# Kernel optimization log

Measured on AMD Instinct MI355X. Metric: run time of the kernel, lower is better.

Reference implementation:

```python
import jax, jax.numpy as jnp
import numpy as np

N = 50000   # nodes
E = 800000  # directed edges
D = 128     # input_channels


def _kaiming(key, shape):
    fan_in = shape[0]
    return jax.random.normal(key, shape, jnp.float32) * np.float32(np.sqrt(2.0 / fan_in))


def setup_inputs():
    key = jax.random.key(0)
    ks = jax.random.split(key, 8)
    x = jax.random.normal(ks[0], (N, D), jnp.float32)
    edge_index = jax.random.randint(ks[1], (2, E), 0, N, dtype=jnp.int32)
    return {
        "x": x,
        "edge_index": edge_index,
        "W_in": _kaiming(ks[2], (D, D)),      "b_in": jnp.zeros((D,), jnp.float32),
        "W1": _kaiming(ks[3], (D, 2 * D)),    "b1": jnp.zeros((2 * D,), jnp.float32),
        "W2": _kaiming(ks[4], (2 * D, D)),    "b2": jnp.zeros((D,), jnp.float32),
        "W3": _kaiming(ks[5], (D, D // 2)),   "b3": jnp.zeros((D // 2,), jnp.float32),
        "W_out": _kaiming(ks[6], (D // 2, 1)), "b_out": jnp.zeros((1,), jnp.float32),
    }


def _gcn_conv(x, src, dst, W, b, n):
    """PyG GCNConv: add self-loops, symmetric D^-1/2 (A+I) D^-1/2 normalization."""
    h = x @ W  # [n, out]
    loop = jnp.arange(n, dtype=src.dtype)
    s = jnp.concatenate([src, loop])  # message sources (x_j)
    d = jnp.concatenate([dst, loop])  # aggregation targets (x_i)
    deg = jax.ops.segment_sum(jnp.ones_like(d, jnp.float32), d, num_segments=n)
    dis = jnp.where(deg > 0, jax.lax.rsqrt(jnp.maximum(deg, 1.0)), 0.0)
    norm = dis[s] * dis[d]  # [E+n]
    msg = h[s] * norm[:, None]  # gather + scale
    out = jax.ops.segment_sum(msg, d, num_segments=n)  # scatter-add
    return out + b


def reference(x, edge_index, W_in, b_in, W1, b1, W2, b2, W3, b3, W_out, b_out):
    src, dst = edge_index[0], edge_index[1]
    n = x.shape[0]
    lrelu = lambda t: jax.nn.leaky_relu(t, 0.01)
    # dropout in eval mode (identity)
    h = lrelu(x @ W_in + b_in)
    h = lrelu(_gcn_conv(h, src, dst, W1, b1, n))
    h = lrelu(_gcn_conv(h, src, dst, W2, b2, n))
    h = lrelu(_gcn_conv(h, src, dst, W3, b3, n))
    return h @ W_out + b_out  # [n, 1]
```

## Files before the change

### kernel.cpp

```cpp
#include <hip/hip_runtime.h>


#define LRELU(v) ((v) > 0.f ? (v) : 0.01f * (v))

typedef __attribute__((ext_vector_type(8))) _Float16 half8;
typedef __attribute__((ext_vector_type(8))) float float8;
typedef __attribute__((ext_vector_type(4))) float floatx4;

constexpr int CAP = 64;

__global__ __launch_bounds__(256) void k_prep(const int* __restrict__ src,
                                              const int* __restrict__ dst,
                                              int* __restrict__ cnt,
                                              unsigned short* __restrict__ pad,
                                              const float* __restrict__ W_in,
                                              const float* __restrict__ W1,
                                              const float* __restrict__ W2,
                                              const float* __restrict__ W3,
                                              _Float16* __restrict__ wt_in,
                                              _Float16* __restrict__ wt1,
                                              _Float16* __restrict__ wt2,
                                              _Float16* __restrict__ wt3,
                                              int E, int PR) {
  const int b = blockIdx.x;
  const int tid = threadIdx.x;
  if (b < 128) {
    const int m = b >> 5;
    const int blk = b & 31;
    const int idx = blk * 256 + tid;
    if (m == 0) {
      for (int i = idx; i < 128 * 128; i += 8192) {
        const int k = i >> 7, f = i & 127;
        wt_in[f * 128 + k] = (_Float16)W_in[i];
      }
    } else if (m == 1) {
      for (int i = idx; i < 128 * 256; i += 8192) {
        const int k = i >> 8, f = i & 255;
        wt1[f * 128 + k] = (_Float16)W1[i];
      }
    } else if (m == 2) {
      for (int i = idx; i < 256 * 128; i += 8192) {
        const int k = i >> 7, f = i & 127;
        wt2[f * 256 + k] = (_Float16)W2[i];
      }
    } else {
      for (int i = idx; i < 128 * 64; i += 8192) {
        const int k = i >> 6, f = i & 63;
        wt3[f * 128 + k] = (_Float16)W3[i];
      }
    }
  } else {
    const int bb = b - 128;
    const int range = bb & 7;
    const int chunk = bb >> 3;
    const int e = chunk * 256 + tid;
    if (e < E) {
      const int d = dst[e];
      if (d / PR == range) {
        const int pos = atomicAdd(&cnt[d], 1);
        if (pos < CAP) pad[(long)d * CAP + pos] = (unsigned short)src[e];
      }
    }
  }
}

template <int K, int F, int EPI, typename IT>
__global__ __launch_bounds__(256) void k_gemm(const IT* __restrict__ X,
                                              const _Float16* __restrict__ Wt,
                                              const float* __restrict__ b,
                                              const int* __restrict__ cnt,
                                              _Float16* __restrict__ out, int M) {
  constexpr int TM = 64;
  constexpr int PAD = 8;
  constexpr int LK = K + PAD;
  constexpr int CW = F / 4;
  constexpr int NT = CW / 16;
  constexpr int NK = K / 32;
  __shared__ _Float16 xs[TM * LK];

  const int m0 = blockIdx.x * TM;
  const int tid = threadIdx.x;
  const int w = tid >> 6;
  const int lane = tid & 63;
  const int m = lane & 15;
  const int q = lane >> 4;

  half8 breg[NT][NK];
#pragma unroll
  for (int t = 0; t < NT; ++t)
#pragma unroll
    for (int kc = 0; kc < NK; ++kc)
      breg[t][kc] =
          *(const half8*)&Wt[(long)(w * CW + t * 16 + m) * K + kc * 32 + q * 8];

  constexpr int CPR = K / 8;
  for (int idx = tid; idx < TM * CPR; idx += 256) {
    const int row = idx / CPR;
    const int kk = idx % CPR;
    const int g = m0 + row;
    half8 h = (half8)(_Float16)0.f;
    if (g < M) {
      if constexpr (sizeof(IT) == 4) {
        const float4* p = (const float4*)&X[(long)g * K + kk * 8];
        float4 a = p[0], c = p[1];
        h[0] = (_Float16)a.x; h[1] = (_Float16)a.y;
        h[2] = (_Float16)a.z; h[3] = (_Float16)a.w;
        h[4] = (_Float16)c.x; h[5] = (_Float16)c.y;
        h[6] = (_Float16)c.z; h[7] = (_Float16)c.w;
      } else {
        h = *(const half8*)&X[(long)g * K + kk * 8];
      }
    }
    *(half8*)&xs[row * LK + kk * 8] = h;
  }
  __syncthreads();

  floatx4 acc[4][NT];
#pragma unroll
  for (int rt = 0; rt < 4; ++rt)
#pragma unroll
    for (int t = 0; t < NT; ++t) acc[rt][t] = (floatx4){0.f, 0.f, 0.f, 0.f};

#pragma unroll
  for (int kc = 0; kc < NK; ++kc) {
    half8 af[4];
#pragma unroll
    for (int rt = 0; rt < 4; ++rt)
      af[rt] = *(const half8*)&xs[(rt * 16 + m) * LK + kc * 32 + q * 8];
#pragma unroll
    for (int rt = 0; rt < 4; ++rt)
#pragma unroll
      for (int t = 0; t < NT; ++t)
        acc[rt][t] = __builtin_amdgcn_mfma_f32_16x16x32_f16(af[rt], breg[t][kc],
                                                            acc[rt][t], 0, 0, 0);
  }

#pragma unroll
  for (int rt = 0; rt < 4; ++rt) {
#pragma unroll
    for (int r = 0; r < 4; ++r) {
      const int row = m0 + rt * 16 + q * 4 + r;
      if (row < M) {
        const float dv = rsqrtf((float)cnt[row] + 1.0f);
#pragma unroll
        for (int t = 0; t < NT; ++t) {
          const int col = w * CW + t * 16 + m;
          float v = acc[rt][t][r];
          if constexpr (EPI == 0) { v += b[col]; v = LRELU(v); v *= dv; }
          if constexpr (EPI == 2) { v *= dv; }
          out[(long)row * F + col] = (_Float16)v;
        }
      }
    }
  }
}

__global__ __launch_bounds__(256) void k_gemm2x(const _Float16* __restrict__ X,
                                                const _Float16* __restrict__ Wt1,
                                                const float* __restrict__ b1,
                                                const _Float16* __restrict__ Wt2,
                                                const int* __restrict__ cnt,
                                                _Float16* __restrict__ out,
                                                int M) {
  constexpr int TM = 64;
  constexpr int LK1 = 128 + 8;
  constexpr int LK2 = 256 + 8;
  __shared__ _Float16 xs[TM * LK1];
  __shared__ _Float16 ys[TM * LK2];

  const int m0 = blockIdx.x * TM;
  const int tid = threadIdx.x;
  const int w = tid >> 6;
  const int lane = tid & 63;
  const int m = lane & 15;
  const int q = lane >> 4;

  for (int idx = tid; idx < TM * 16; idx += 256) {
    const int row = idx >> 4;
    const int kk = idx & 15;
    const int g = m0 + row;
    half8 h = (half8)(_Float16)0.f;
    if (g < M) h = *(const half8*)&X[(long)g * 128 + kk * 8];
    *(half8*)&xs[row * LK1 + kk * 8] = h;
  }

  half8 breg1[4][4];
#pragma unroll
  for (int t = 0; t < 4; ++t)
#pragma unroll
    for (int kc = 0; kc < 4; ++kc)
      breg1[t][kc] =
          *(const half8*)&Wt1[(long)(w * 64 + t * 16 + m) * 128 + kc * 32 + q * 8];

  __syncthreads();

  floatx4 acc1[4][4];
#pragma unroll
  for (int rt = 0; rt < 4; ++rt)
#pragma unroll
    for (int t = 0; t < 4; ++t) acc1[rt][t] = (floatx4){0.f, 0.f, 0.f, 0.f};

#pragma unroll
  for (int kc = 0; kc < 4; ++kc) {
    half8 af[4];
#pragma unroll
    for (int rt = 0; rt < 4; ++rt)
      af[rt] = *(const half8*)&xs[(rt * 16 + m) * LK1 + kc * 32 + q * 8];
#pragma unroll
    for (int rt = 0; rt < 4; ++rt)
#pragma unroll
      for (int t = 0; t < 4; ++t)
        acc1[rt][t] = __builtin_amdgcn_mfma_f32_16x16x32_f16(af[rt], breg1[t][kc],
                                                             acc1[rt][t], 0, 0, 0);
  }

#pragma unroll
  for (int rt = 0; rt < 4; ++rt) {
#pragma unroll
    for (int r = 0; r < 4; ++r) {
      const int row = rt * 16 + q * 4 + r;
#pragma unroll
      for (int t = 0; t < 4; ++t) {
        const int col = w * 64 + t * 16 + m;
        float v = acc1[rt][t][r] + b1[col];
        ys[row * LK2 + col] = (_Float16)LRELU(v);
      }
    }
  }

  half8 breg2[2][8];
#pragma unroll
  for (int t = 0; t < 2; ++t)
#pragma unroll
    for (int kc = 0; kc < 8; ++kc)
      breg2[t][kc] =
          *(const half8*)&Wt2[(long)(w * 32 + t * 16 + m) * 256 + kc * 32 + q * 8];

  __syncthreads();

  floatx4 acc2[4][2];
#pragma unroll
  for (int rt = 0; rt < 4; ++rt)
#pragma unroll
    for (int t = 0; t < 2; ++t) acc2[rt][t] = (floatx4){0.f, 0.f, 0.f, 0.f};

#pragma unroll
  for (int kc = 0; kc < 8; ++kc) {
    half8 af[4];
#pragma unroll
    for (int rt = 0; rt < 4; ++rt)
      af[rt] = *(const half8*)&ys[(rt * 16 + m) * LK2 + kc * 32 + q * 8];
#pragma unroll
    for (int rt = 0; rt < 4; ++rt)
#pragma unroll
      for (int t = 0; t < 2; ++t)
        acc2[rt][t] = __builtin_amdgcn_mfma_f32_16x16x32_f16(af[rt], breg2[t][kc],
                                                             acc2[rt][t], 0, 0, 0);
  }

#pragma unroll
  for (int rt = 0; rt < 4; ++rt) {
#pragma unroll
    for (int r = 0; r < 4; ++r) {
      const int row = m0 + rt * 16 + q * 4 + r;
      if (row < M) {
        const float dv = rsqrtf((float)cnt[row] + 1.0f);
#pragma unroll
        for (int t = 0; t < 2; ++t) {
          const int col = w * 32 + t * 16 + m;
          out[(long)row * 128 + col] = (_Float16)(acc2[rt][t][r] * dv);
        }
      }
    }
  }
}

template <int F, int MODE>
__global__ __launch_bounds__(256) void k_agg(const _Float16* __restrict__ G,
                                             const unsigned short* __restrict__ pad,
                                             const int* __restrict__ cnt,
                                             const float* __restrict__ b,
                                             const float* __restrict__ Wout,
                                             const float* __restrict__ bout,
                                             void* __restrict__ out, int N) {
  const int w = threadIdx.x >> 6;
  const int lane = threadIdx.x & 63;
  const int c = lane & 7;
  const int j = lane >> 3;
  const int n = j >> 2;
  const int jj = j & 3;
  const int i0 = blockIdx.x * 8 + w * 2;
  int i = i0 + n;
  const bool valid = (i < N);
  if (!valid) i = N - 1;
  const int col0 = (F == 128) ? ((int)blockIdx.y << 6) : 0;

  const _Float16* gbase = G + col0 + c * 8;
  const int cn = min(cnt[i], CAP);
  const unsigned short* plist = pad + (long)i * CAP;

  float8 acc = {0.f, 0.f, 0.f, 0.f, 0.f, 0.f, 0.f, 0.f};
  if (jj == 0)
    acc = __builtin_convertvector(*(const half8*)(gbase + (long)i * F), float8);
  for (int e = jj; e < cn; e += 4) {
    const int s = plist[e];
    acc += __builtin_convertvector(*(const half8*)(gbase + (long)s * F), float8);
  }
#pragma unroll
  for (int k = 0; k < 8; ++k) {
    acc[k] += __shfl_xor(acc[k], 8);
    acc[k] += __shfl_xor(acc[k], 16);
  }

  const float dv = rsqrtf((float)cnt[i] + 1.0f);
  if constexpr (MODE == 2) {
    float p = 0.f;
#pragma unroll
    for (int k = 0; k < 8; ++k) {
      const int col = c * 8 + k;
      float v = acc[k] * dv + b[col];
      v = LRELU(v);
      p += v * Wout[col];
    }
    p += __shfl_xor(p, 1);
    p += __shfl_xor(p, 2);
    p += __shfl_xor(p, 4);
    if (valid && jj == 0 && c == 0) ((float*)out)[i] = p + bout[0];
  } else {
    if (valid && jj == 0) {
      half8 hv;
#pragma unroll
      for (int k = 0; k < 8; ++k) {
        float v = acc[k] * dv;
        if constexpr (MODE == 1) { v += b[col0 + c * 8 + k]; v = LRELU(v); }
        hv[k] = (_Float16)v;
      }
      *(half8*)&((_Float16*)out)[(long)i * F + col0 + c * 8] = hv;
    }
  }
}


extern "C" void kernel_launch(void* const* d_in, const int* in_sizes, int n_in,
                              void* d_out, int out_size, void* d_ws, size_t ws_size,
                              hipStream_t stream) {
  const float* x     = (const float*)d_in[0];
  const int* eidx    = (const int*)d_in[1];
  const float* W_in  = (const float*)d_in[2];
  const float* b_in  = (const float*)d_in[3];
  const float* W1    = (const float*)d_in[4];
  const float* b1    = (const float*)d_in[5];
  const float* W2    = (const float*)d_in[6];
  const float* b2    = (const float*)d_in[7];
  const float* W3    = (const float*)d_in[8];
  const float* b3    = (const float*)d_in[9];
  const float* W_out = (const float*)d_in[10];
  const float* b_out = (const float*)d_in[11];
  float* out = (float*)d_out;

  const int N = in_sizes[0] / 128;
  const int E = in_sizes[1] / 2;
  const int* src = eidx;
  const int* dst = eidx + E;
  const int PR = (N + 7) / 8;

  size_t off = 0;
  char* base = (char*)d_ws;
  auto alloc = [&](size_t bytes) -> void* {
    void* p = base + off;
    off = (off + bytes + 255) & ~(size_t)255;
    return p;
  };
  int* cnt            = (int*)alloc((size_t)N * sizeof(int));
  unsigned short* pad = (unsigned short*)alloc((size_t)N * CAP * 2);
  _Float16* wt_in     = (_Float16*)alloc((size_t)128 * 128 * 2);
  _Float16* wt1       = (_Float16*)alloc((size_t)256 * 128 * 2);
  _Float16* wt2       = (_Float16*)alloc((size_t)128 * 256 * 2);
  _Float16* wt3       = (_Float16*)alloc((size_t)64 * 128 * 2);
  _Float16* buf1      = (_Float16*)alloc((size_t)N * 128 * 2);
  _Float16* buf2      = (_Float16*)alloc((size_t)N * 128 * 2);
  _Float16* buf3      = (_Float16*)alloc((size_t)N * 64 * 2);

  hipMemsetAsync(cnt, 0, (size_t)N * sizeof(int), stream);

  const int gE = (E + 255) / 256;
  const int gRows = (N + 63) / 64;
  const int gAggP = (N + 7) / 8;

  k_prep<<<128 + 8 * gE, 256, 0, stream>>>(src, dst, cnt, pad,
                                           W_in, W1, W2, W3,
                                           wt_in, wt1, wt2, wt3, E, PR);

  k_gemm<128, 128, 0, float><<<gRows, 256, 0, stream>>>(x, wt_in, b_in, cnt,
                                                        buf1, N);
  k_agg<128, 0><<<dim3(gAggP, 2), 256, 0, stream>>>(buf1, pad, cnt, nullptr,
                                                    nullptr, nullptr, buf2, N);
  k_gemm2x<<<gRows, 256, 0, stream>>>(buf2, wt1, b1, wt2, cnt, buf1, N);
  k_agg<128, 1><<<dim3(gAggP, 2), 256, 0, stream>>>(buf1, pad, cnt, b2,
                                                    nullptr, nullptr, buf2, N);
  k_gemm<128, 64, 2, _Float16><<<gRows, 256, 0, stream>>>(buf2, wt3, nullptr,
                                                          cnt, buf3, N);
  k_agg<64, 2><<<gAggP, 256, 0, stream>>>(buf3, pad, cnt, b3,
                                          W_out, b_out, out, N);
}
```

Before: 273.4 us.

## Fuse whole GCN pipeline into one persistent cooperative kernel with grid syncs

```diff
diff --git a/kernel.cpp b/kernel.cpp
--- a/kernel.cpp
+++ b/kernel.cpp
@@ -1,4 +1,7 @@
 #include <hip/hip_runtime.h>
+#include <hip/hip_cooperative_groups.h>
+
+namespace cg = cooperative_groups;
 
 
 #define LRELU(v) ((v) > 0.f ? (v) : 0.01f * (v))
@@ -8,6 +11,470 @@
 typedef __attribute__((ext_vector_type(4))) float floatx4;
 
 constexpr int CAP = 64;
+
+template <int K, int F, int EPI, typename IT>
+__device__ __forceinline__ void gemm_tile(const IT* __restrict__ X,
+                                          const _Float16* __restrict__ Wt,
+                                          const float* __restrict__ bias,
+                                          const int* __restrict__ cnt,
+                                          _Float16* __restrict__ out, int M,
+                                          int tile, _Float16* __restrict__ xs) {
+  constexpr int TM = 64;
+  constexpr int PAD = 8;
+  constexpr int LK = K + PAD;
+  constexpr int CW = F / 4;
+  constexpr int NT = CW / 16;
+  constexpr int NK = K / 32;
+
+  const int m0 = tile * TM;
+  const int tid = threadIdx.x;
+  const int w = tid >> 6;
+  const int lane = tid & 63;
+  const int m = lane & 15;
+  const int q = lane >> 4;
+
+  half8 breg[NT][NK];
+#pragma unroll
+  for (int t = 0; t < NT; ++t)
+#pragma unroll
+    for (int kc = 0; kc < NK; ++kc)
+      breg[t][kc] =
+          *(const half8*)&Wt[(long)(w * CW + t * 16 + m) * K + kc * 32 + q * 8];
+
+  constexpr int CPR = K / 8;
+  for (int idx = tid; idx < TM * CPR; idx += 256) {
+    const int row = idx / CPR;
+    const int kk = idx % CPR;
+    const int g = m0 + row;
+    half8 h = (half8)(_Float16)0.f;
+    if (g < M) {
+      if constexpr (sizeof(IT) == 4) {
+        const float4* p = (const float4*)&X[(long)g * K + kk * 8];
+        float4 a = p[0], cc = p[1];
+        h[0] = (_Float16)a.x; h[1] = (_Float16)a.y;
+        h[2] = (_Float16)a.z; h[3] = (_Float16)a.w;
+        h[4] = (_Float16)cc.x; h[5] = (_Float16)cc.y;
+        h[6] = (_Float16)cc.z; h[7] = (_Float16)cc.w;
+      } else {
+        h = *(const half8*)&X[(long)g * K + kk * 8];
+      }
+    }
+    *(half8*)&xs[row * LK + kk * 8] = h;
+  }
+  __syncthreads();
+
+  floatx4 acc[4][NT];
+#pragma unroll
+  for (int rt = 0; rt < 4; ++rt)
+#pragma unroll
+    for (int t = 0; t < NT; ++t) acc[rt][t] = (floatx4){0.f, 0.f, 0.f, 0.f};
+
+#pragma unroll
+  for (int kc = 0; kc < NK; ++kc) {
+    half8 af[4];
+#pragma unroll
+    for (int rt = 0; rt < 4; ++rt)
+      af[rt] = *(const half8*)&xs[(rt * 16 + m) * LK + kc * 32 + q * 8];
+#pragma unroll
+    for (int rt = 0; rt < 4; ++rt)
+#pragma unroll
+      for (int t = 0; t < NT; ++t)
+        acc[rt][t] = __builtin_amdgcn_mfma_f32_16x16x32_f16(af[rt], breg[t][kc],
+                                                            acc[rt][t], 0, 0, 0);
+  }
+
+#pragma unroll
+  for (int rt = 0; rt < 4; ++rt) {
+#pragma unroll
+    for (int r = 0; r < 4; ++r) {
+      const int row = m0 + rt * 16 + q * 4 + r;
+      if (row < M) {
+        float dv = 1.f;
+        if constexpr (EPI == 0 || EPI == 2) dv = rsqrtf((float)cnt[row] + 1.0f);
+#pragma unroll
+        for (int t = 0; t < NT; ++t) {
+          const int col = w * CW + t * 16 + m;
+          float v = acc[rt][t][r];
+          if constexpr (EPI == 0) { v += bias[col]; v = LRELU(v); v *= dv; }
+          if constexpr (EPI == 1) { v += bias[col]; v = LRELU(v); }
+          if constexpr (EPI == 2) { v *= dv; }
+          out[(long)row * F + col] = (_Float16)v;
+        }
+      }
+    }
+  }
+}
+
+__device__ __forceinline__ void gemm2x_tile(const _Float16* __restrict__ X,
+                                            const _Float16* __restrict__ Wt1,
+                                            const float* __restrict__ b1,
+                                            const _Float16* __restrict__ Wt2,
+                                            const int* __restrict__ cnt,
+                                            _Float16* __restrict__ out, int M,
+                                            int tile, _Float16* __restrict__ xs,
+                                            _Float16* __restrict__ ys) {
+  constexpr int LK1 = 128 + 8;
+  constexpr int LK2 = 256 + 8;
+
+  const int m0 = tile * 64;
+  const int tid = threadIdx.x;
+  const int w = tid >> 6;
+  const int lane = tid & 63;
+  const int m = lane & 15;
+  const int q = lane >> 4;
+
+  for (int idx = tid; idx < 64 * 16; idx += 256) {
+    const int row = idx >> 4;
+    const int kk = idx & 15;
+    const int g = m0 + row;
+    half8 h = (half8)(_Float16)0.f;
+    if (g < M) h = *(const half8*)&X[(long)g * 128 + kk * 8];
+    *(half8*)&xs[row * LK1 + kk * 8] = h;
+  }
+
+  half8 breg1[4][4];
+#pragma unroll
+  for (int t = 0; t < 4; ++t)
+#pragma unroll
+    for (int kc = 0; kc < 4; ++kc)
+      breg1[t][kc] =
+          *(const half8*)&Wt1[(long)(w * 64 + t * 16 + m) * 128 + kc * 32 + q * 8];
+
+  __syncthreads();
+
+  floatx4 acc1[4][4];
+#pragma unroll
+  for (int rt = 0; rt < 4; ++rt)
+#pragma unroll
+    for (int t = 0; t < 4; ++t) acc1[rt][t] = (floatx4){0.f, 0.f, 0.f, 0.f};
+
+#pragma unroll
+  for (int kc = 0; kc < 4; ++kc) {
+    half8 af[4];
+#pragma unroll
+    for (int rt = 0; rt < 4; ++rt)
+      af[rt] = *(const half8*)&xs[(rt * 16 + m) * LK1 + kc * 32 + q * 8];
+#pragma unroll
+    for (int rt = 0; rt < 4; ++rt)
+#pragma unroll
+      for (int t = 0; t < 4; ++t)
+        acc1[rt][t] = __builtin_amdgcn_mfma_f32_16x16x32_f16(af[rt], breg1[t][kc],
+                                                             acc1[rt][t], 0, 0, 0);
+  }
+
+#pragma unroll
+  for (int rt = 0; rt < 4; ++rt) {
+#pragma unroll
+    for (int r = 0; r < 4; ++r) {
+      const int row = rt * 16 + q * 4 + r;
+#pragma unroll
+      for (int t = 0; t < 4; ++t) {
+        const int col = w * 64 + t * 16 + m;
+        float v = acc1[rt][t][r] + b1[col];
+        ys[row * LK2 + col] = (_Float16)LRELU(v);
+      }
+    }
+  }
+
+  half8 breg2[2][8];
+#pragma unroll
+  for (int t = 0; t < 2; ++t)
+#pragma unroll
+    for (int kc = 0; kc < 8; ++kc)
+      breg2[t][kc] =
+          *(const half8*)&Wt2[(long)(w * 32 + t * 16 + m) * 256 + kc * 32 + q * 8];
+
+  __syncthreads();
+
+  floatx4 acc2[4][2];
+#pragma unroll
+  for (int rt = 0; rt < 4; ++rt)
+#pragma unroll
+    for (int t = 0; t < 2; ++t) acc2[rt][t] = (floatx4){0.f, 0.f, 0.f, 0.f};
+
+#pragma unroll
+  for (int kc = 0; kc < 8; ++kc) {
+    half8 af[4];
+#pragma unroll
+    for (int rt = 0; rt < 4; ++rt)
+      af[rt] = *(const half8*)&ys[(rt * 16 + m) * LK2 + kc * 32 + q * 8];
+#pragma unroll
+    for (int rt = 0; rt < 4; ++rt)
+#pragma unroll
+      for (int t = 0; t < 2; ++t)
+        acc2[rt][t] = __builtin_amdgcn_mfma_f32_16x16x32_f16(af[rt], breg2[t][kc],
+                                                             acc2[rt][t], 0, 0, 0);
+  }
+
+#pragma unroll
+  for (int rt = 0; rt < 4; ++rt) {
+#pragma unroll
+    for (int r = 0; r < 4; ++r) {
+      const int row = m0 + rt * 16 + q * 4 + r;
+      if (row < M) {
+        const float dv = rsqrtf((float)cnt[row] + 1.0f);
+#pragma unroll
+        for (int t = 0; t < 2; ++t) {
+          const int col = w * 32 + t * 16 + m;
+          out[(long)row * 128 + col] = (_Float16)(acc2[rt][t][r] * dv);
+        }
+      }
+    }
+  }
+}
+
+__device__ __forceinline__ void agg128_pre(const _Float16* __restrict__ G,
+                                           const unsigned short* __restrict__ pad,
+                                           const int* __restrict__ cnt,
+                                           _Float16* __restrict__ out, int N,
+                                           int nb) {
+  const int w = threadIdx.x >> 6;
+  const int lane = threadIdx.x & 63;
+  const int c = lane & 15;
+  const int jj = lane >> 4;
+  const int ng = (N + 3) >> 2;
+  for (int t = blockIdx.x; t < ng; t += nb) {
+    int i = t * 4 + w;
+    const bool valid = (i < N);
+    if (!valid) i = N - 1;
+    const int cni = cnt[i];
+    const int cn = min(cni, CAP);
+    const float dvi = rsqrtf((float)cni + 1.f);
+    const _Float16* gb = G + c * 8;
+    const unsigned short* pl = pad + (long)i * CAP;
+
+    float8 a0 = {0.f, 0.f, 0.f, 0.f, 0.f, 0.f, 0.f, 0.f};
+    float8 a1 = a0, a2 = a0, a3 = a0;
+    if (jj == 0) {
+      float8 f = __builtin_convertvector(*(const half8*)(gb + (long)i * 128), float8);
+#pragma unroll
+      for (int k = 0; k < 8; ++k) a0[k] = f[k] * dvi;
+    }
+    int e = jj;
+    for (; e + 12 < cn; e += 16) {
+      const int s0 = pl[e], s1 = pl[e + 4], s2 = pl[e + 8], s3 = pl[e + 12];
+      const float d0 = rsqrtf((float)cnt[s0] + 1.f);
+      const float d1 = rsqrtf((float)cnt[s1] + 1.f);
+      const float d2 = rsqrtf((float)cnt[s2] + 1.f);
+      const float d3 = rsqrtf((float)cnt[s3] + 1.f);
+      float8 f0 = __builtin_convertvector(*(const half8*)(gb + (long)s0 * 128), float8);
+      float8 f1 = __builtin_convertvector(*(const half8*)(gb + (long)s1 * 128), float8);
+      float8 f2 = __builtin_convertvector(*(const half8*)(gb + (long)s2 * 128), float8);
+      float8 f3 = __builtin_convertvector(*(const half8*)(gb + (long)s3 * 128), float8);
+#pragma unroll
+      for (int k = 0; k < 8; ++k) {
+        a0[k] += f0[k] * d0;
+        a1[k] += f1[k] * d1;
+        a2[k] += f2[k] * d2;
+        a3[k] += f3[k] * d3;
+      }
+    }
+    for (; e < cn; e += 4) {
+      const int s = pl[e];
+      const float d = rsqrtf((float)cnt[s] + 1.f);
+      float8 f = __builtin_convertvector(*(const half8*)(gb + (long)s * 128), float8);
+#pragma unroll
+      for (int k = 0; k < 8; ++k) a0[k] += f[k] * d;
+    }
+#pragma unroll
+    for (int k = 0; k < 8; ++k) a0[k] += a1[k] + a2[k] + a3[k];
+#pragma unroll
+    for (int k = 0; k < 8; ++k) {
+      a0[k] += __shfl_xor(a0[k], 16);
+      a0[k] += __shfl_xor(a0[k], 32);
+    }
+    if (valid && jj == 0) {
+      half8 hv;
+#pragma unroll
+      for (int k = 0; k < 8; ++k) hv[k] = (_Float16)(a0[k] * dvi);
+      *(half8*)&out[(long)i * 128 + c * 8] = hv;
+    }
+  }
+}
+
+__device__ __forceinline__ void agg128_post(const _Float16* __restrict__ G,
+                                            const unsigned short* __restrict__ pad,
+                                            const int* __restrict__ cnt,
+                                            const float* __restrict__ bias,
+                                            _Float16* __restrict__ out, int N,
+                                            int nb) {
+  const int w = threadIdx.x >> 6;
+  const int lane = threadIdx.x & 63;
+  const int c = lane & 15;
+  const int jj = lane >> 4;
+  const int ng = (N + 3) >> 2;
+  for (int t = blockIdx.x; t < ng; t += nb) {
+    int i = t * 4 + w;
+    const bool valid = (i < N);
+    if (!valid) i = N - 1;
+    const int cni = cnt[i];
+    const int cn = min(cni, CAP);
+    const float dvi = rsqrtf((float)cni + 1.f);
+    const _Float16* gb = G + c * 8;
+    const unsigned short* pl = pad + (long)i * CAP;
+
+    float8 a0 = {0.f, 0.f, 0.f, 0.f, 0.f, 0.f, 0.f, 0.f};
+    float8 a1 = a0, a2 = a0, a3 = a0;
+    if (jj == 0)
+      a0 = __builtin_convertvector(*(const half8*)(gb + (long)i * 128), float8);
+    int e = jj;
+    for (; e + 12 < cn; e += 16) {
+      const int s0 = pl[e], s1 = pl[e + 4], s2 = pl[e + 8], s3 = pl[e + 12];
+      a0 += __builtin_convertvector(*(const half8*)(gb + (long)s0 * 128), float8);
+      a1 += __builtin_convertvector(*(const half8*)(gb + (long)s1 * 128), float8);
+      a2 += __builtin_convertvector(*(const half8*)(gb + (long)s2 * 128), float8);
+      a3 += __builtin_convertvector(*(const half8*)(gb + (long)s3 * 128), float8);
+    }
+    for (; e < cn; e += 4) {
+      const int s = pl[e];
+      a0 += __builtin_convertvector(*(const half8*)(gb + (long)s * 128), float8);
+    }
+    a0 += a1 + a2 + a3;
+#pragma unroll
+    for (int k = 0; k < 8; ++k) {
+      a0[k] += __shfl_xor(a0[k], 16);
+      a0[k] += __shfl_xor(a0[k], 32);
+    }
+    if (valid && jj == 0) {
+      half8 hv;
+#pragma unroll
+      for (int k = 0; k < 8; ++k) {
+        float v = a0[k] * dvi + bias[c * 8 + k];
+        hv[k] = (_Float16)LRELU(v);
+      }
+      *(half8*)&out[(long)i * 128 + c * 8] = hv;
+    }
+  }
+}
+
+__device__ __forceinline__ void agg_final(const _Float16* __restrict__ G,
+                                          const unsigned short* __restrict__ pad,
+                                          const int* __restrict__ cnt,
+                                          const float* __restrict__ b3,
+                                          const float* __restrict__ Wout,
+                                          const float* __restrict__ bout,
+                                          float* __restrict__ out, int N, int nb) {
+  const int w = threadIdx.x >> 6;
+  const int lane = threadIdx.x & 63;
+  const int c = lane & 7;
+  const int j = lane >> 3;
+  const int n = j >> 2;
+  const int jj = j & 3;
+  const int ng = (N + 7) >> 3;
+  for (int t = blockIdx.x; t < ng; t += nb) {
+    int i = t * 8 + w * 2 + n;
+    const bool valid = (i < N);
+    if (!valid) i = N - 1;
+    const int cni = cnt[i];
+    const int cn = min(cni, CAP);
+    const float dvi = rsqrtf((float)cni + 1.f);
+    const _Float16* gb = G + c * 8;
+    const unsigned short* pl = pad + (long)i * CAP;
+
+    float8 a0 = {0.f, 0.f, 0.f, 0.f, 0.f, 0.f, 0.f, 0.f};
+    float8 a1 = a0;
+    if (jj == 0)
+      a0 = __builtin_convertvector(*(const half8*)(gb + (long)i * 64), float8);
+    int e = jj;
+    for (; e + 4 < cn; e += 8) {
+      const int s0 = pl[e], s1 = pl[e + 4];
+      a0 += __builtin_convertvector(*(const half8*)(gb + (long)s0 * 64), float8);
+      a1 += __builtin_convertvector(*(const half8*)(gb + (long)s1 * 64), float8);
+    }
+    if (e < cn)
+      a0 += __builtin_convertvector(*(const half8*)(gb + (long)pl[e] * 64), float8);
+    a0 += a1;
+#pragma unroll
+    for (int k = 0; k < 8; ++k) {
+      a0[k] += __shfl_xor(a0[k], 8);
+      a0[k] += __shfl_xor(a0[k], 16);
+    }
+    float p = 0.f;
+#pragma unroll
+    for (int k = 0; k < 8; ++k) {
+      const int col = c * 8 + k;
+      float v = a0[k] * dvi + b3[col];
+      v = LRELU(v);
+      p += v * Wout[col];
+    }
+    p += __shfl_xor(p, 1);
+    p += __shfl_xor(p, 2);
+    p += __shfl_xor(p, 4);
+    if (valid && jj == 0 && c == 0) out[i] = p + bout[0];
+  }
+}
+
+__global__ __launch_bounds__(256, 2) void k_gcn(
+    const float* __restrict__ x, const int* __restrict__ src,
+    const int* __restrict__ dst, const float* __restrict__ W_in,
+    const float* __restrict__ b_in, const float* __restrict__ W1,
+    const float* __restrict__ b1, const float* __restrict__ W2,
+    const float* __restrict__ b2, const float* __restrict__ W3,
+    const float* __restrict__ b3, const float* __restrict__ W_out,
+    const float* __restrict__ b_out, float* __restrict__ out,
+    int* __restrict__ cnt, unsigned short* __restrict__ pad,
+    _Float16* __restrict__ wt_in, _Float16* __restrict__ wt1,
+    _Float16* __restrict__ wt2, _Float16* __restrict__ wt3,
+    _Float16* __restrict__ buf1, _Float16* __restrict__ buf2,
+    _Float16* __restrict__ buf3, int N, int E, int PR) {
+  __shared__ _Float16 smem[64 * 136 + 64 * 264];
+  cg::grid_group grid = cg::this_grid();
+  const int nb = gridDim.x;
+  const int b = blockIdx.x;
+  const int tid = threadIdx.x;
+  const int gid = b * 256 + tid;
+  const int gs = nb * 256;
+
+  for (int i = gid; i < N; i += gs) cnt[i] = 0;
+  for (int i = gid; i < 128 * 128; i += gs)
+    wt_in[(i & 127) * 128 + (i >> 7)] = (_Float16)W_in[i];
+  for (int i = gid; i < 128 * 256; i += gs)
+    wt1[(i & 255) * 128 + (i >> 8)] = (_Float16)W1[i];
+  for (int i = gid; i < 256 * 128; i += gs)
+    wt2[(i & 127) * 256 + (i >> 7)] = (_Float16)W2[i];
+  for (int i = gid; i < 128 * 64; i += gs)
+    wt3[(i & 63) * 128 + (i >> 6)] = (_Float16)W3[i];
+  grid.sync();
+
+  const int gE = (E + 255) >> 8;
+  for (int ch = b; ch < 8 * gE; ch += nb) {
+    const int range = ch & 7;
+    const int e = (ch >> 3) * 256 + tid;
+    if (e < E) {
+      const int d = dst[e];
+      if ((unsigned)(d - range * PR) < (unsigned)PR) {
+        const int pos = atomicAdd(&cnt[d], 1);
+        if (pos < CAP) pad[(long)d * CAP + pos] = (unsigned short)src[e];
+      }
+    }
+  }
+  const int ntile = (N + 63) >> 6;
+  for (int t = b; t < ntile; t += nb) {
+    gemm_tile<128, 128, 1, float>(x, wt_in, b_in, nullptr, buf1, N, t, smem);
+    __syncthreads();
+  }
+  grid.sync();
+
+  agg128_pre(buf1, pad, cnt, buf2, N, nb);
+  grid.sync();
+
+  for (int t = b; t < ntile; t += nb) {
+    gemm2x_tile(buf2, wt1, b1, wt2, cnt, buf1, N, t, smem, smem + 64 * 136);
+    __syncthreads();
+  }
+  grid.sync();
+
+  agg128_post(buf1, pad, cnt, b2, buf2, N, nb);
+  grid.sync();
+
+  for (int t = b; t < ntile; t += nb) {
+    gemm_tile<128, 64, 2, _Float16>(buf2, wt3, nullptr, cnt, buf3, N, t, smem);
+    __syncthreads();
+  }
+  grid.sync();
+
+  agg_final(buf3, pad, cnt, b3, W_out, b_out, out, N, nb);
+}
 
 __global__ __launch_bounds__(256) void k_prep(const int* __restrict__ src,
                                               const int* __restrict__ dst,
@@ -70,89 +537,8 @@
                                               const float* __restrict__ b,
                                               const int* __restrict__ cnt,
                                               _Float16* __restrict__ out, int M) {
-  constexpr int TM = 64;
-  constexpr int PAD = 8;
-  constexpr int LK = K + PAD;
-  constexpr int CW = F / 4;
-  constexpr int NT = CW / 16;
-  constexpr int NK = K / 32;
-  __shared__ _Float16 xs[TM * LK];
-
-  const int m0 = blockIdx.x * TM;
-  const int tid = threadIdx.x;
-  const int w = tid >> 6;
-  const int lane = tid & 63;
-  const int m = lane & 15;
-  const int q = lane >> 4;
-
-  half8 breg[NT][NK];
-#pragma unroll
-  for (int t = 0; t < NT; ++t)
-#pragma unroll
-    for (int kc = 0; kc < NK; ++kc)
-      breg[t][kc] =
-          *(const half8*)&Wt[(long)(w * CW + t * 16 + m) * K + kc * 32 + q * 8];
-
-  constexpr int CPR = K / 8;
-  for (int idx = tid; idx < TM * CPR; idx += 256) {
-    const int row = idx / CPR;
-    const int kk = idx % CPR;
-    const int g = m0 + row;
-    half8 h = (half8)(_Float16)0.f;
-    if (g < M) {
-      if constexpr (sizeof(IT) == 4) {
-        const float4* p = (const float4*)&X[(long)g * K + kk * 8];
-        float4 a = p[0], c = p[1];
-        h[0] = (_Float16)a.x; h[1] = (_Float16)a.y;
-        h[2] = (_Float16)a.z; h[3] = (_Float16)a.w;
-        h[4] = (_Float16)c.x; h[5] = (_Float16)c.y;
-        h[6] = (_Float16)c.z; h[7] = (_Float16)c.w;
-      } else {
-        h = *(const half8*)&X[(long)g * K + kk * 8];
-      }
-    }
-    *(half8*)&xs[row * LK + kk * 8] = h;
-  }
-  __syncthreads();
-
-  floatx4 acc[4][NT];
-#pragma unroll
-  for (int rt = 0; rt < 4; ++rt)
-#pragma unroll
-    for (int t = 0; t < NT; ++t) acc[rt][t] = (floatx4){0.f, 0.f, 0.f, 0.f};
-
-#pragma unroll
-  for (int kc = 0; kc < NK; ++kc) {
-    half8 af[4];
-#pragma unroll
-    for (int rt = 0; rt < 4; ++rt)
-      af[rt] = *(const half8*)&xs[(rt * 16 + m) * LK + kc * 32 + q * 8];
-#pragma unroll
-    for (int rt = 0; rt < 4; ++rt)
-#pragma unroll
-      for (int t = 0; t < NT; ++t)
-        acc[rt][t] = __builtin_amdgcn_mfma_f32_16x16x32_f16(af[rt], breg[t][kc],
-                                                            acc[rt][t], 0, 0, 0);
-  }
-
-#pragma unroll
-  for (int rt = 0; rt < 4; ++rt) {
-#pragma unroll
-    for (int r = 0; r < 4; ++r) {
-      const int row = m0 + rt * 16 + q * 4 + r;
-      if (row < M) {
-        const float dv = rsqrtf((float)cnt[row] + 1.0f);
-#pragma unroll
-        for (int t = 0; t < NT; ++t) {
-          const int col = w * CW + t * 16 + m;
-          float v = acc[rt][t][r];
-          if constexpr (EPI == 0) { v += b[col]; v = LRELU(v); v *= dv; }
-          if constexpr (EPI == 2) { v *= dv; }
-          out[(long)row * F + col] = (_Float16)v;
-        }
-      }
-    }
-  }
+  __shared__ _Float16 xs[64 * (K + 8)];
+  gemm_tile<K, F, EPI, IT>(X, Wt, b, cnt, out, M, blockIdx.x, xs);
 }
 
 __global__ __launch_bounds__(256) void k_gemm2x(const _Float16* __restrict__ X,
@@ -162,117 +548,9 @@
                                                 const int* __restrict__ cnt,
                                                 _Float16* __restrict__ out,
                                                 int M) {
-  constexpr int TM = 64;
-  constexpr int LK1 = 128 + 8;
-  constexpr int LK2 = 256 + 8;
-  __shared__ _Float16 xs[TM * LK1];
-  __shared__ _Float16 ys[TM * LK2];
-
-  const int m0 = blockIdx.x * TM;
-  const int tid = threadIdx.x;
-  const int w = tid >> 6;
-  const int lane = tid & 63;
-  const int m = lane & 15;
-  const int q = lane >> 4;
-
-  for (int idx = tid; idx < TM * 16; idx += 256) {
-    const int row = idx >> 4;
-    const int kk = idx & 15;
-    const int g = m0 + row;
-    half8 h = (half8)(_Float16)0.f;
-    if (g < M) h = *(const half8*)&X[(long)g * 128 + kk * 8];
-    *(half8*)&xs[row * LK1 + kk * 8] = h;
-  }
-
-  half8 breg1[4][4];
-#pragma unroll
-  for (int t = 0; t < 4; ++t)
-#pragma unroll
-    for (int kc = 0; kc < 4; ++kc)
-      breg1[t][kc] =
-          *(const half8*)&Wt1[(long)(w * 64 + t * 16 + m) * 128 + kc * 32 + q * 8];
-
-  __syncthreads();
-
-  floatx4 acc1[4][4];
-#pragma unroll
-  for (int rt = 0; rt < 4; ++rt)
-#pragma unroll
-    for (int t = 0; t < 4; ++t) acc1[rt][t] = (floatx4){0.f, 0.f, 0.f, 0.f};
-
-#pragma unroll
-  for (int kc = 0; kc < 4; ++kc) {
-    half8 af[4];
-#pragma unroll
-    for (int rt = 0; rt < 4; ++rt)
-      af[rt] = *(const half8*)&xs[(rt * 16 + m) * LK1 + kc * 32 + q * 8];
-#pragma unroll
-    for (int rt = 0; rt < 4; ++rt)
-#pragma unroll
-      for (int t = 0; t < 4; ++t)
-        acc1[rt][t] = __builtin_amdgcn_mfma_f32_16x16x32_f16(af[rt], breg1[t][kc],
-                                                             acc1[rt][t], 0, 0, 0);
-  }
-
-#pragma unroll
-  for (int rt = 0; rt < 4; ++rt) {
-#pragma unroll
-    for (int r = 0; r < 4; ++r) {
-      const int row = rt * 16 + q * 4 + r;
-#pragma unroll
-      for (int t = 0; t < 4; ++t) {
-        const int col = w * 64 + t * 16 + m;
-        float v = acc1[rt][t][r] + b1[col];
-        ys[row * LK2 + col] = (_Float16)LRELU(v);
-      }
-    }
-  }
-
-  half8 breg2[2][8];
-#pragma unroll
-  for (int t = 0; t < 2; ++t)
-#pragma unroll
-    for (int kc = 0; kc < 8; ++kc)
-      breg2[t][kc] =
-          *(const half8*)&Wt2[(long)(w * 32 + t * 16 + m) * 256 + kc * 32 + q * 8];
-
-  __syncthreads();
-
-  floatx4 acc2[4][2];
-#pragma unroll
-  for (int rt = 0; rt < 4; ++rt)
-#pragma unroll
-    for (int t = 0; t < 2; ++t) acc2[rt][t] = (floatx4){0.f, 0.f, 0.f, 0.f};
-
-#pragma unroll
-  for (int kc = 0; kc < 8; ++kc) {
-    half8 af[4];
-#pragma unroll
-    for (int rt = 0; rt < 4; ++rt)
-      af[rt] = *(const half8*)&ys[(rt * 16 + m) * LK2 + kc * 32 + q * 8];
-#pragma unroll
-    for (int rt = 0; rt < 4; ++rt)
-#pragma unroll
-      for (int t = 0; t < 2; ++t)
-        acc2[rt][t] = __builtin_amdgcn_mfma_f32_16x16x32_f16(af[rt], breg2[t][kc],
-                                                             acc2[rt][t], 0, 0, 0);
-  }
-
-#pragma unroll
-  for (int rt = 0; rt < 4; ++rt) {
-#pragma unroll
-    for (int r = 0; r < 4; ++r) {
-      const int row = m0 + rt * 16 + q * 4 + r;
-      if (row < M) {
-        const float dv = rsqrtf((float)cnt[row] + 1.0f);
-#pragma unroll
-        for (int t = 0; t < 2; ++t) {
-          const int col = w * 32 + t * 16 + m;
-          out[(long)row * 128 + col] = (_Float16)(acc2[rt][t][r] * dv);
-        }
-      }
-    }
-  }
+  __shared__ _Float16 xs[64 * 136];
+  __shared__ _Float16 ys[64 * 264];
+  gemm2x_tile(X, Wt1, b1, Wt2, cnt, out, M, blockIdx.x, xs, ys);
 }
 
 template <int F, int MODE>
@@ -358,11 +636,11 @@
   const float* b_out = (const float*)d_in[11];
   float* out = (float*)d_out;
 
-  const int N = in_sizes[0] / 128;
-  const int E = in_sizes[1] / 2;
+  int N = in_sizes[0] / 128;
+  int E = in_sizes[1] / 2;
   const int* src = eidx;
   const int* dst = eidx + E;
-  const int PR = (N + 7) / 8;
+  int PR = (N + 7) / 8;
 
   size_t off = 0;
   char* base = (char*)d_ws;
@@ -381,25 +659,53 @@
   _Float16* buf2      = (_Float16*)alloc((size_t)N * 128 * 2);
   _Float16* buf3      = (_Float16*)alloc((size_t)N * 64 * 2);
 
-  hipMemsetAsync(cnt, 0, (size_t)N * sizeof(int), stream);
-
-  const int gE = (E + 255) / 256;
-  const int gRows = (N + 63) / 64;
-  const int gAggP = (N + 7) / 8;
-
-  k_prep<<<128 + 8 * gE, 256, 0, stream>>>(src, dst, cnt, pad,
-                                           W_in, W1, W2, W3,
-                                           wt_in, wt1, wt2, wt3, E, PR);
-
-  k_gemm<128, 128, 0, float><<<gRows, 256, 0, stream>>>(x, wt_in, b_in, cnt,
-                                                        buf1, N);
-  k_agg<128, 0><<<dim3(gAggP, 2), 256, 0, stream>>>(buf1, pad, cnt, nullptr,
-                                                    nullptr, nullptr, buf2, N);
-  k_gemm2x<<<gRows, 256, 0, stream>>>(buf2, wt1, b1, wt2, cnt, buf1, N);
-  k_agg<128, 1><<<dim3(gAggP, 2), 256, 0, stream>>>(buf1, pad, cnt, b2,
-                                                    nullptr, nullptr, buf2, N);
-  k_gemm<128, 64, 2, _Float16><<<gRows, 256, 0, stream>>>(buf2, wt3, nullptr,
-                                                          cnt, buf3, N);
-  k_agg<64, 2><<<gAggP, 256, 0, stream>>>(buf3, pad, cnt, b3,
-                                          W_out, b_out, out, N);
-}
+  static int s_grid = 0;
+  if (s_grid == 0) {
+    int mb = 0;
+    if (hipOccupancyMaxActiveBlocksPerMultiprocessor(&mb, k_gcn, 256, 0) !=
+            hipSuccess ||
+        mb < 1)
+      mb = 2;
+    int ncu = 0;
+    if (hipDeviceGetAttribute(&ncu, hipDeviceAttributeMultiprocessorCount, 0) !=
+            hipSuccess ||
+        ncu < 1)
+      ncu = 256;
+    long g = (long)mb * ncu;
+    if (g > 1024) g = 1024;
+    g &= ~(long)7;
+    if (g < 8) g = 8;
+    s_grid = (int)g;
+  }
+
+  void* args[] = {(void*)&x,     (void*)&src,   (void*)&dst,  (void*)&W_in,
+                  (void*)&b_in,  (void*)&W1,    (void*)&b1,   (void*)&W2,
+                  (void*)&b2,    (void*)&W3,    (void*)&b3,   (void*)&W_out,
+                  (void*)&b_out, (void*)&out,   (void*)&cnt,  (void*)&pad,
+                  (void*)&wt_in, (void*)&wt1,   (void*)&wt2,  (void*)&wt3,
+                  (void*)&buf1,  (void*)&buf2,  (void*)&buf3, (void*)&N,
+                  (void*)&E,     (void*)&PR};
+
+  hipError_t rc = hipLaunchCooperativeKernel((const void*)k_gcn, dim3(s_grid),
+                                             dim3(256), args, 0, stream);
+  if (rc != hipSuccess) {
+    (void)hipGetLastError();
+    hipMemsetAsync(cnt, 0, (size_t)N * sizeof(int), stream);
+    const int gE = (E + 255) / 256;
+    const int gRows = (N + 63) / 64;
+    const int gAggP = (N + 7) / 8;
+    k_prep<<<128 + 8 * gE, 256, 0, stream>>>(src, dst, cnt, pad, W_in, W1, W2,
+                                             W3, wt_in, wt1, wt2, wt3, E, PR);
+    k_gemm<128, 128, 0, float><<<gRows, 256, 0, stream>>>(x, wt_in, b_in, cnt,
+                                                          buf1, N);
+    k_agg<128, 0><<<dim3(gAggP, 2), 256, 0, stream>>>(buf1, pad, cnt, nullptr,
+                                                      nullptr, nullptr, buf2, N);
+    k_gemm2x<<<gRows, 256, 0, stream>>>(buf2, wt1, b1, wt2, cnt, buf1, N);
+    k_agg<128, 1><<<dim3(gAggP, 2), 256, 0, stream>>>(buf1, pad, cnt, b2,
+                                                      nullptr, nullptr, buf2, N);
+    k_gemm<128, 64, 2, _Float16><<<gRows, 256, 0, stream>>>(buf2, wt3, nullptr,
+                                                            cnt, buf3, N);
+    k_agg<64, 2><<<gAggP, 256, 0, stream>>>(buf3, pad, cnt, b3, W_out, b_out,
+                                            out, N);
+  }
+}
```

Measured after the change: 762.7 us. 179% more time.
